# Optimization experiments

Hardware: AMD Instinct MI355X
Metric: run time of the kernel (lower is better)

Reference implementation:

```python
import jax, jax.numpy as jnp
import numpy as np

B, N, DIM, H = 32, 480, 1024, 16


def setup_inputs() -> dict:
    key = jax.random.key(0)
    ks = jax.random.split(key, 7)
    s = 0.02
    return {
        "q": jax.random.normal(ks[0], (B, N, DIM), jnp.float32),
        "Wq": jax.random.normal(ks[1], (DIM, DIM), jnp.float32) * s,
        "Wk": jax.random.normal(ks[2], (DIM, DIM), jnp.float32) * s,
        "Wv": jax.random.normal(ks[3], (DIM, DIM), jnp.float32) * s,
        "pe": jax.random.normal(ks[4], (480, 480), jnp.float32),
        "Wo": jax.random.normal(ks[5], (DIM, DIM), jnp.float32) * s,
        "bo": jnp.zeros((DIM,), jnp.float32),
    }


def reference(q, Wq, Wk, Wv, pe, Wo, bo):
    b, n, dim = q.shape
    h = H
    d = dim // h
    scale = d ** -0.5
    # self-attention: k = v = q (pre-projection)
    qp = (q @ Wq.T).reshape(b, n, h, d).transpose(0, 2, 1, 3)  # b h n d
    kp = (q @ Wk.T).reshape(b, n, h, d).transpose(0, 2, 1, 3)
    vp = (q @ Wv.T).reshape(b, n, h, d).transpose(0, 2, 1, 3)
    dots = jnp.einsum("bhid,bhjd->bhij", qp, kp) * scale
    dots = dots + pe[:n, :n]  # learned additive positional bias
    attn = jax.nn.softmax(dots, axis=-1)
    out = jnp.einsum("bhij,bhjd->bhid", attn, vp)
    out = out.transpose(0, 2, 1, 3).reshape(b, n, dim)
    return out @ Wo.T + bo
```

## Files before the change

### kernel.cpp

```cpp
#include <hip/hip_runtime.h>
#include <hip/hip_bf16.h>
#include <stdint.h>

#define B_   32
#define N_   480
#define DIM_ 1024
#define H_   16
#define D_   64
#define M_   (B_*N_)
#define BH_  (B_*H_)

typedef __bf16 bf16;
typedef __bf16 bf16x4 __attribute__((ext_vector_type(4)));
typedef __bf16 bf16x8 __attribute__((ext_vector_type(8)));
typedef short  short4v __attribute__((ext_vector_type(4)));
typedef float  f32x4  __attribute__((ext_vector_type(4)));

__device__ __forceinline__ void gld_lds16(const void* g, void* l) {
    using GP = const __attribute__((address_space(1))) unsigned int*;
    using LP = __attribute__((address_space(3))) unsigned int*;
    __builtin_amdgcn_global_load_lds((GP)(uintptr_t)g, (LP)(unsigned int)(uintptr_t)l, 16, 0, 0);
}

__global__ void cvt4(const float* __restrict__ in, bf16* __restrict__ out, int n4) {
    int i = blockIdx.x * 256 + threadIdx.x;
    if (i >= n4) return;
    float4 v = ((const float4*)in)[i];
    bf16x4 o = { (bf16)v.x, (bf16)v.y, (bf16)v.z, (bf16)v.w };
    ((bf16x4*)out)[i] = o;
}

__global__ void cvtW(const float* __restrict__ Wq, const float* __restrict__ Wk,
                     const float* __restrict__ Wv, const float* __restrict__ Wo,
                     bf16* __restrict__ Wcat, bf16* __restrict__ Wob) {
    int i = blockIdx.x * 256 + threadIdx.x;
    const float* src; bf16* dst;
    switch (blockIdx.y) {
        case 0: src = Wq; dst = Wcat;                break;
        case 1: src = Wk; dst = Wcat + DIM_*DIM_;    break;
        case 2: src = Wv; dst = Wcat + 2*DIM_*DIM_;  break;
        default: src = Wo; dst = Wob;                break;
    }
    float4 v = ((const float4*)src)[i];
    bf16x4 o = { (bf16)v.x, (bf16)v.y, (bf16)v.z, (bf16)v.w };
    ((bf16x4*)dst)[i] = o;
}

#define GEMM_PRE()                                                            \
    const int tid  = threadIdx.x;                                             \
    const int lane = tid & 63;                                                \
    const int wid  = tid >> 6;                                                \
    const int wm   = wid & 1, wn = wid >> 1;                                  \
    const int m0   = blockIdx.y * 128;                                        \
    const int n0   = blockIdx.x * 128;                                        \
    const int lm   = lane & 15, lq = lane >> 4;                               \
    const int aLane = (lane >> 3) * 1024 + (((lane & 7) ^ (lane >> 3)) & 7) * 8; \
    const bf16* Asrc = A  + (m0 + wid*32) * 1024 + aLane;                     \
    const bf16* Bsrc = Bw + (n0 + wid*32) * 1024 + aLane;                     \
    bf16* AsDst = As + (wid*32)*64;                                           \
    bf16* BsDst = Bs + (wid*32)*64;                                           \
    int rowA[4], rowB[4];                                                     \
    _Pragma("unroll") for (int m = 0; m < 4; ++m) rowA[m] = (wm*64 + m*16 + lm)*64; \
    _Pragma("unroll") for (int n = 0; n < 4; ++n) rowB[n] = (wn*64 + n*16 + lm)*64; \
    const int sw = lm & 7;                                                    \
    int phys[2];                                                              \
    phys[0] = ((lq)     ^ sw) * 8;                                            \
    phys[1] = ((4 + lq) ^ sw) * 8;

#define GEMM_KLOOP(FIRST, SECOND)                                             \
    for (int k0 = 0; k0 < 1024; k0 += 64) {                                   \
        _Pragma("unroll") for (int j = 0; j < 4; ++j) {                       \
            gld_lds16(Asrc + k0 + j*8192, AsDst + j*512);                     \
            gld_lds16(Bsrc + k0 + j*8192, BsDst + j*512);                     \
        }                                                                     \
        __syncthreads();                                                      \
        _Pragma("unroll") for (int ks = 0; ks < 2; ++ks) {                    \
            bf16x8 af[4], bfr[4];                                             \
            _Pragma("unroll") for (int m = 0; m < 4; ++m)                     \
                af[m]  = *(const bf16x8*)&As[rowA[m] + phys[ks]];             \
            _Pragma("unroll") for (int n = 0; n < 4; ++n)                     \
                bfr[n] = *(const bf16x8*)&Bs[rowB[n] + phys[ks]];             \
            _Pragma("unroll") for (int m = 0; m < 4; ++m)                     \
                _Pragma("unroll") for (int n = 0; n < 4; ++n)                 \
                    acc[m][n] = __builtin_amdgcn_mfma_f32_16x16x32_bf16(      \
                        FIRST, SECOND, acc[m][n], 0, 0, 0);                   \
        }                                                                     \
        __syncthreads();                                                      \
    }

__global__ __launch_bounds__(256) void gemm_qkv(const bf16* __restrict__ A, const bf16* __restrict__ Bw,
                                                bf16* __restrict__ Qp, bf16* __restrict__ Kp,
                                                bf16* __restrict__ Vt) {
    __shared__ bf16 As[128*64];
    __shared__ bf16 Bs[128*64];
    GEMM_PRE();
    const int part = n0 >> 10;
    f32x4 acc[4][4] = {};

    if (part != 2) {
        GEMM_KLOOP(af[m], bfr[n]);
        bf16* dst = (part == 0) ? Qp : Kp;
        int hh[4], dd[4];
#pragma unroll
        for (int n = 0; n < 4; ++n) {
            int rem = (n0 + wn*64 + n*16 + lm) & 1023;
            hh[n] = rem >> 6; dd[n] = rem & 63;
        }
#pragma unroll
        for (int m = 0; m < 4; ++m) {
#pragma unroll
            for (int r = 0; r < 4; ++r) {
                int gm = m0 + wm*64 + m*16 + lq*4 + r;
                int b  = gm / 480;
                int nn = gm - b*480;
#pragma unroll
                for (int n = 0; n < 4; ++n)
                    dst[((b*16 + hh[n])*480 + nn)*64 + dd[n]] = (bf16)acc[m][n][r];
            }
        }
    } else {
        GEMM_KLOOP(bfr[n], af[m]);
#pragma unroll
        for (int m = 0; m < 4; ++m) {
            int gmBase = m0 + wm*64 + m*16;
            int b  = gmBase / 480;
            int nn = gmBase - b*480 + lm;
#pragma unroll
            for (int n = 0; n < 4; ++n)
#pragma unroll
                for (int r = 0; r < 4; ++r) {
                    int rem = (n0 + wn*64 + n*16 + lq*4 + r) & 1023;
                    int h = rem >> 6, d = rem & 63;
                    Vt[((b*16 + h)*64 + d)*480 + nn] = (bf16)acc[m][n][r];
                }
        }
    }
}

#define KT 96
#define KS_LD 72
#define VS_LD 104
__global__ __launch_bounds__(320) void attn(const bf16* __restrict__ Qp, const bf16* __restrict__ Kp,
                                            const bf16* __restrict__ Vt, const float* __restrict__ pe,
                                            bf16* __restrict__ O) {
    __shared__ bf16 Ks[KT*KS_LD];
    __shared__ bf16 Vs[64*VS_LD];
    const int tid  = threadIdx.x;
    const int lane = tid & 63, wid = tid >> 6;
    const int bh   = blockIdx.y;
    const int b    = bh >> 4, h = bh & 15;
    const int qblk = blockIdx.x * 80;
    const int lm   = lane & 15, lq = lane >> 4;
    const int qbase = bh * (N_ * 64);

    bf16x8 qb[2];
#pragma unroll
    for (int ks = 0; ks < 2; ++ks)
        qb[ks] = *(const bf16x8*)&Qp[qbase + (qblk + wid*16 + lm)*64 + ks*32 + lq*8];
    const float* peRow = pe + (qblk + wid*16 + lm)*480;

    f32x4 ot[4] = {};
    float lsum = 0.f;

    for (int kt = 0; kt < 5; ++kt) {
        __syncthreads();
        for (int c = tid; c < 768; c += 320) {
            int row = c >> 3, of = (c & 7) * 8;
            *(uint4*)&Ks[row*KS_LD + of] = *(const uint4*)&Kp[qbase + (kt*KT + row)*64 + of];
        }
        for (int c = tid; c < 768; c += 320) {
            int row = c / 12, of = (c % 12) * 8;
            *(uint4*)&Vs[row*VS_LD + of] = *(const uint4*)&Vt[qbase + row*480 + kt*KT + of];
        }
        __syncthreads();

        short4v pb[6];
#pragma unroll
        for (int mf = 0; mf < 6; ++mf) {
            f32x4 s = {};
#pragma unroll
            for (int ks = 0; ks < 2; ++ks) {
                bf16x8 ka = *(const bf16x8*)&Ks[(mf*16 + lm)*KS_LD + ks*32 + lq*8];
                s = __builtin_amdgcn_mfma_f32_16x16x32_bf16(ka, qb[ks], s, 0, 0, 0);
            }
            bf16x4 pv;
#pragma unroll
            for (int r = 0; r < 4; ++r) {
                float e = __expf(s[r] * 0.125f + peRow[kt*KT + mf*16 + lq*4 + r]);
                lsum += e;
                pv[r] = (bf16)e;
            }
            pb[mf] = __builtin_bit_cast(short4v, pv);
        }

#pragma unroll
        for (int df = 0; df < 4; ++df)
#pragma unroll
            for (int mf = 0; mf < 6; ++mf) {
                short4v va = *(const short4v*)&Vs[(df*16 + lm)*VS_LD + mf*16 + lq*4];
                ot[df] = __builtin_amdgcn_mfma_f32_16x16x16bf16_1k(va, pb[mf], ot[df], 0, 0, 0);
            }
    }

    lsum += __shfl_xor(lsum, 16);
    lsum += __shfl_xor(lsum, 32);
    float rl = 1.f / lsum;

    __syncthreads();
    bf16* Os = Ks;
#pragma unroll
    for (int df = 0; df < 4; ++df)
#pragma unroll
        for (int r = 0; r < 4; ++r)
            Os[(wid*16 + lm)*KS_LD + df*16 + lq*4 + r] = (bf16)(ot[df][r] * rl);
    __syncthreads();
    for (int c = tid; c < 640; c += 320) {
        int row = c >> 3, d0 = (c & 7) * 8;
        uint4 u = *(const uint4*)&Os[row*KS_LD + d0];
        *(uint4*)&O[(b*480 + qblk + row)*1024 + h*64 + d0] = u;
    }
}

__global__ __launch_bounds__(256) void gemm_out(const bf16* __restrict__ A, const bf16* __restrict__ Bw,
                                                const float* __restrict__ bo, float* __restrict__ out) {
    __shared__ bf16 As[128*64];
    __shared__ bf16 Bs[128*64];
    GEMM_PRE();
    f32x4 acc[4][4] = {};
    GEMM_KLOOP(af[m], bfr[n]);
#pragma unroll
    for (int m = 0; m < 4; ++m)
#pragma unroll
        for (int n = 0; n < 4; ++n)
#pragma unroll
            for (int r = 0; r < 4; ++r) {
                int gm = m0 + wm*64 + m*16 + lq*4 + r;
                int gn = n0 + wn*64 + n*16 + lm;
                out[gm*1024 + gn] = acc[m][n][r] + bo[gn];
            }
}

extern "C" void kernel_launch(void* const* d_in, const int* in_sizes, int n_in,
                              void* d_out, int out_size, void* d_ws, size_t ws_size,
                              hipStream_t stream) {
    const float* q  = (const float*)d_in[0];
    const float* Wq = (const float*)d_in[1];
    const float* Wk = (const float*)d_in[2];
    const float* Wv = (const float*)d_in[3];
    const float* pe = (const float*)d_in[4];
    const float* Wo = (const float*)d_in[5];
    const float* bo = (const float*)d_in[6];
    float* out = (float*)d_out;

    char* ws = (char*)d_ws;
    bf16* Abf  = (bf16*)(ws);
    bf16* Wcat = (bf16*)(ws + 31457280);
    bf16* Wob  = (bf16*)(ws + 31457280 + 6291456);
    bf16* Qp   = (bf16*)(ws + 39845888);
    bf16* Kp   = (bf16*)(ws + 71303168);
    bf16* Vt   = (bf16*)(ws + 102760448);

    cvt4<<<(M_*DIM_/4 + 255)/256, 256, 0, stream>>>(q, Abf, M_*DIM_/4);
    cvtW<<<dim3(DIM_*DIM_/4/256, 4), 256, 0, stream>>>(Wq, Wk, Wv, Wo, Wcat, Wob);

    gemm_qkv<<<dim3(24, 120), 256, 0, stream>>>(Abf, Wcat, Qp, Kp, Vt);
    attn<<<dim3(6, 512), 320, 0, stream>>>(Qp, Kp, Vt, pe, Abf);
    gemm_out<<<dim3(8, 120), 256, 0, stream>>>(Abf, Wob, bo, out);
}
```

Before: 410.7 us.

## Prefetch next K/V tile into registers and swizzle LDS layout in attention

The attention kernel now loads the next K and V tiles into registers while MFMA work runs on the current tile, then writes them to LDS after a barrier. Padded LDS rows are replaced with XOR-swizzled layouts to avoid bank conflicts, and the positional-bias reads become vectorized float4 loads. The prefetch adds register pressure at 320 threads, and V loads are clamped at the tile edge, which relies on index masking being correct.

Measured after the change: 509.2 us. 1.24x slower.

```diff
diff --git a/kernel.cpp b/kernel.cpp
--- a/kernel.cpp
+++ b/kernel.cpp
@@ -138,13 +138,14 @@
 }
 
 #define KT 96
-#define KS_LD 72
-#define VS_LD 104
+#define OS_LD 72
 __global__ __launch_bounds__(320) void attn(const bf16* __restrict__ Qp, const bf16* __restrict__ Kp,
                                             const bf16* __restrict__ Vt, const float* __restrict__ pe,
                                             bf16* __restrict__ O) {
-    __shared__ bf16 Ks[KT*KS_LD];
-    __shared__ bf16 Vs[64*VS_LD];
+    __shared__ bf16 Ks[KT*64];
+    __shared__ bf16 Vs[64*128];
+    char* KsB = (char*)Ks;
+    char* VsB = (char*)Vs;
     const int tid  = threadIdx.x;
     const int lane = tid & 63, wid = tid >> 6;
     const int bh   = blockIdx.y;
@@ -153,26 +154,66 @@
     const int lm   = lane & 15, lq = lane >> 4;
     const int qbase = bh * (N_ * 64);
 
+    const bool kHas2 = tid < 128;
+    int kLds[3];
+#pragma unroll
+    for (int i = 0; i < 3; ++i) {
+        int id = tid + i*320, r = id >> 3, c = id & 7;
+        kLds[i] = r*128 + ((c ^ (r & 7)) << 4);
+    }
+    const bool vHas3 = tid < 64;
+    int vLds[4], vColB[4], vRowB[4];
+#pragma unroll
+    for (int i = 0; i < 4; ++i) {
+        int id = tid + i*320, r = id >> 4, c = id & 15;
+        vLds[i]  = r*256 + (((c & 8) | ((c & 7) ^ (r & 7))) << 4);
+        vColB[i] = c * 8;
+        vRowB[i] = (bh*64 + r) * 480;
+    }
+
     bf16x8 qb[2];
 #pragma unroll
     for (int ks = 0; ks < 2; ++ks)
         qb[ks] = *(const bf16x8*)&Qp[qbase + (qblk + wid*16 + lm)*64 + ks*32 + lq*8];
-    const float* peRow = pe + (qblk + wid*16 + lm)*480;
+    const float* peP = pe + (qblk + wid*16 + lm)*480 + lq*4;
+
+    int kOff[2];
+#pragma unroll
+    for (int ks = 0; ks < 2; ++ks) kOff[ks] = ((ks*4 + lq) ^ (lm & 7)) << 4;
+    int vOff[6];
+#pragma unroll
+    for (int mf = 0; mf < 6; ++mf) {
+        int c = 2*mf + (lq >> 1);
+        vOff[mf] = (((c & 8) | ((c & 7) ^ (lm & 7))) << 4) + (lq & 1)*8;
+    }
+
+    uint4 kreg[3], vreg[4];
+#define LOAD_TILE(T)                                                          \
+    {   const char* kg = (const char*)Kp + (size_t)(qbase + (T)*KT*64)*2;     \
+        kreg[0] = *(const uint4*)(kg + tid*16);                               \
+        kreg[1] = *(const uint4*)(kg + tid*16 + 5120);                        \
+        if (kHas2) kreg[2] = *(const uint4*)(kg + tid*16 + 10240);            \
+        _Pragma("unroll") for (int i = 0; i < 4; ++i)                         \
+            if (i < 3 || vHas3) {                                             \
+                int key = (T)*KT + vColB[i]; if (key > 472) key = 472;        \
+                vreg[i] = *(const uint4*)((const char*)Vt + (size_t)(vRowB[i] + key)*2); \
+            } }
+
+    LOAD_TILE(0);
 
     f32x4 ot[4] = {};
     float lsum = 0.f;
 
     for (int kt = 0; kt < 5; ++kt) {
+        if (kt) __syncthreads();
+        *(uint4*)(KsB + kLds[0]) = kreg[0];
+        *(uint4*)(KsB + kLds[1]) = kreg[1];
+        if (kHas2) *(uint4*)(KsB + kLds[2]) = kreg[2];
+#pragma unroll
+        for (int i = 0; i < 4; ++i)
+            if (i < 3 || vHas3) *(uint4*)(VsB + vLds[i]) = vreg[i];
         __syncthreads();
-        for (int c = tid; c < 768; c += 320) {
-            int row = c >> 3, of = (c & 7) * 8;
-            *(uint4*)&Ks[row*KS_LD + of] = *(const uint4*)&Kp[qbase + (kt*KT + row)*64 + of];
-        }
-        for (int c = tid; c < 768; c += 320) {
-            int row = c / 12, of = (c % 12) * 8;
-            *(uint4*)&Vs[row*VS_LD + of] = *(const uint4*)&Vt[qbase + row*480 + kt*KT + of];
-        }
-        __syncthreads();
+        if (kt < 4) LOAD_TILE(kt + 1);
 
         short4v pb[6];
 #pragma unroll
@@ -180,13 +221,14 @@
             f32x4 s = {};
 #pragma unroll
             for (int ks = 0; ks < 2; ++ks) {
-                bf16x8 ka = *(const bf16x8*)&Ks[(mf*16 + lm)*KS_LD + ks*32 + lq*8];
+                bf16x8 ka = *(const bf16x8*)(KsB + (mf*16 + lm)*128 + kOff[ks]);
                 s = __builtin_amdgcn_mfma_f32_16x16x32_bf16(ka, qb[ks], s, 0, 0, 0);
             }
+            f32x4 pe4 = *(const f32x4*)(peP + kt*KT + mf*16);
             bf16x4 pv;
 #pragma unroll
             for (int r = 0; r < 4; ++r) {
-                float e = __expf(s[r] * 0.125f + peRow[kt*KT + mf*16 + lq*4 + r]);
+                float e = __expf(s[r] * 0.125f + pe4[r]);
                 lsum += e;
                 pv[r] = (bf16)e;
             }
@@ -194,13 +236,16 @@
         }
 
 #pragma unroll
-        for (int df = 0; df < 4; ++df)
+        for (int df = 0; df < 4; ++df) {
+            const char* vrow = VsB + (df*16 + lm)*256;
 #pragma unroll
             for (int mf = 0; mf < 6; ++mf) {
-                short4v va = *(const short4v*)&Vs[(df*16 + lm)*VS_LD + mf*16 + lq*4];
+                short4v va = *(const short4v*)(vrow + vOff[mf]);
                 ot[df] = __builtin_amdgcn_mfma_f32_16x16x16bf16_1k(va, pb[mf], ot[df], 0, 0, 0);
             }
-    }
+        }
+    }
+#undef LOAD_TILE
 
     lsum += __shfl_xor(lsum, 16);
     lsum += __shfl_xor(lsum, 32);
@@ -212,11 +257,11 @@
     for (int df = 0; df < 4; ++df)
 #pragma unroll
         for (int r = 0; r < 4; ++r)
-            Os[(wid*16 + lm)*KS_LD + df*16 + lq*4 + r] = (bf16)(ot[df][r] * rl);
+            Os[(wid*16 + lm)*OS_LD + df*16 + lq*4 + r] = (bf16)(ot[df][r] * rl);
     __syncthreads();
     for (int c = tid; c < 640; c += 320) {
         int row = c >> 3, d0 = (c & 7) * 8;
-        uint4 u = *(const uint4*)&Os[row*KS_LD + d0];
+        uint4 u = *(const uint4*)&Os[row*OS_LD + d0];
         *(uint4*)&O[(b*480 + qblk + row)*1024 + h*64 + d0] = u;
     }
 }
```

## Load attention K/V tiles via direct global-to-LDS with XOR swizzle

Applied to the files above, without the earlier changes.

Replaces the register-staged K and V tile copies in the attention kernel with global_load_lds direct transfers, and drops the padded LDS layouts in favour of XOR-swizzled ones so the MFMA reads stay free of bank conflicts. The positional bias is now read as one float4 per fragment instead of four scalar loads, and the PV MFMAs are interleaved with the softmax per key fragment rather than run after all six fragments. This removes VGPR round trips and address arithmetic on the load path. The price is more complex swizzle indexing, and V columns past 11 are clamped, which loads redundant data.

New measurement: 393.6 us. 4.2% less time.

```diff
diff --git a/kernel.cpp b/kernel.cpp
--- a/kernel.cpp
+++ b/kernel.cpp
@@ -138,13 +138,12 @@
 }
 
 #define KT 96
-#define KS_LD 72
-#define VS_LD 104
+#define OS_LD 72
 __global__ __launch_bounds__(320) void attn(const bf16* __restrict__ Qp, const bf16* __restrict__ Kp,
                                             const bf16* __restrict__ Vt, const float* __restrict__ pe,
                                             bf16* __restrict__ O) {
-    __shared__ bf16 Ks[KT*KS_LD];
-    __shared__ bf16 Vs[64*VS_LD];
+    __shared__ bf16 Ks[KT*64];
+    __shared__ bf16 Vs[64*128];
     const int tid  = threadIdx.x;
     const int lane = tid & 63, wid = tid >> 6;
     const int bh   = blockIdx.y;
@@ -153,53 +152,70 @@
     const int lm   = lane & 15, lq = lane >> 4;
     const int qbase = bh * (N_ * 64);
 
+    const int kROff = (lane >> 3)*64 + ((lane & 7) ^ (lane >> 3))*8;
+
     bf16x8 qb[2];
 #pragma unroll
     for (int ks = 0; ks < 2; ++ks)
         qb[ks] = *(const bf16x8*)&Qp[qbase + (qblk + wid*16 + lm)*64 + ks*32 + lq*8];
-    const float* peRow = pe + (qblk + wid*16 + lm)*480;
+    const float* peP = pe + (qblk + wid*16 + lm)*480 + lq*4;
+
+    int kOff[2];
+#pragma unroll
+    for (int ks = 0; ks < 2; ++ks) kOff[ks] = ((ks*4 + lq) ^ (lm & 7)) << 4;
 
     f32x4 ot[4] = {};
     float lsum = 0.f;
 
     for (int kt = 0; kt < 5; ++kt) {
         __syncthreads();
-        for (int c = tid; c < 768; c += 320) {
-            int row = c >> 3, of = (c & 7) * 8;
-            *(uint4*)&Ks[row*KS_LD + of] = *(const uint4*)&Kp[qbase + (kt*KT + row)*64 + of];
-        }
-        for (int c = tid; c < 768; c += 320) {
-            int row = c / 12, of = (c % 12) * 8;
-            *(uint4*)&Vs[row*VS_LD + of] = *(const uint4*)&Vt[qbase + row*480 + kt*KT + of];
+#pragma unroll
+        for (int i = 0; i < 6; ++i) {
+            int j = wid + 5*i;
+            if (j < 28) {
+                if (j < 12) {
+                    gld_lds16(Kp + qbase + kt*(KT*64) + j*512 + kROff,
+                              (char*)Ks + j*1024);
+                } else {
+                    int jv = j - 12;
+                    int r  = jv*4 + (lane >> 4);
+                    int p  = lane & 15;
+                    int c  = (p & 8) | ((p & 7) ^ (r & 7));
+                    if (c > 11) c = 11;
+                    gld_lds16(Vt + (size_t)(bh*64 + r)*480 + kt*KT + c*8,
+                              (char*)Vs + jv*1024);
+                }
+            }
         }
         __syncthreads();
 
-        short4v pb[6];
+        const char* KsB = (const char*)Ks;
+        const char* VsB = (const char*)Vs;
 #pragma unroll
         for (int mf = 0; mf < 6; ++mf) {
             f32x4 s = {};
 #pragma unroll
             for (int ks = 0; ks < 2; ++ks) {
-                bf16x8 ka = *(const bf16x8*)&Ks[(mf*16 + lm)*KS_LD + ks*32 + lq*8];
+                bf16x8 ka = *(const bf16x8*)(KsB + (mf*16 + lm)*128 + kOff[ks]);
                 s = __builtin_amdgcn_mfma_f32_16x16x32_bf16(ka, qb[ks], s, 0, 0, 0);
             }
+            f32x4 pe4 = *(const f32x4*)(peP + kt*KT + mf*16);
             bf16x4 pv;
 #pragma unroll
             for (int r = 0; r < 4; ++r) {
-                float e = __expf(s[r] * 0.125f + peRow[kt*KT + mf*16 + lq*4 + r]);
+                float e = __expf(s[r] * 0.125f + pe4[r]);
                 lsum += e;
                 pv[r] = (bf16)e;
             }
-            pb[mf] = __builtin_bit_cast(short4v, pv);
-        }
-
-#pragma unroll
-        for (int df = 0; df < 4; ++df)
-#pragma unroll
-            for (int mf = 0; mf < 6; ++mf) {
-                short4v va = *(const short4v*)&Vs[(df*16 + lm)*VS_LD + mf*16 + lq*4];
-                ot[df] = __builtin_amdgcn_mfma_f32_16x16x16bf16_1k(va, pb[mf], ot[df], 0, 0, 0);
-            }
+            short4v pb = __builtin_bit_cast(short4v, pv);
+            int c = 2*mf + (lq >> 1);
+            int vOff = (((c & 8) | ((c & 7) ^ (lm & 7))) << 4) + (lq & 1)*8;
+#pragma unroll
+            for (int df = 0; df < 4; ++df) {
+                short4v va = *(const short4v*)(VsB + (df*16 + lm)*256 + vOff);
+                ot[df] = __builtin_amdgcn_mfma_f32_16x16x16bf16_1k(va, pb, ot[df], 0, 0, 0);
+            }
+        }
     }
 
     lsum += __shfl_xor(lsum, 16);
@@ -212,11 +228,11 @@
     for (int df = 0; df < 4; ++df)
 #pragma unroll
         for (int r = 0; r < 4; ++r)
-            Os[(wid*16 + lm)*KS_LD + df*16 + lq*4 + r] = (bf16)(ot[df][r] * rl);
+            Os[(wid*16 + lm)*OS_LD + df*16 + lq*4 + r] = (bf16)(ot[df][r] * rl);
     __syncthreads();
     for (int c = tid; c < 640; c += 320) {
         int row = c >> 3, d0 = (c & 7) * 8;
-        uint4 u = *(const uint4*)&Os[row*KS_LD + d0];
+        uint4 u = *(const uint4*)&Os[row*OS_LD + d0];
         *(uint4*)&O[(b*480 + qblk + row)*1024 + h*64 + d0] = u;
     }
 }
```
